# Optimization experiments

Measured on AMD Instinct MI355X. Metric: run time of the kernel, lower is better.

## Reference

```python
import jax, jax.numpy as jnp
import numpy as np

B, C, H, W, HEADS, S = 8, 512, 32, 32, 8, 77
CH = C // HEADS  # per-head channels = 64
GROUPS = 32      # GroupNorm32


def setup_inputs() -> dict:
    key = jax.random.key(0)
    ks = jax.random.split(key, 6)
    s = 0.02
    return {
        "x": jax.random.normal(ks[0], (B, C, H, W), jnp.float32),
        "encoder_out": jax.random.normal(ks[1], (B, C, S), jnp.float32),
        "capt_attn_mask": jax.random.bernoulli(ks[2], 0.9, (B, S)),
        "norm_scale": jnp.ones((C,), jnp.float32),
        "norm_bias": jnp.zeros((C,), jnp.float32),
        "qkv_w": jax.random.normal(ks[3], (3 * C, C), jnp.float32) * s,
        "qkv_b": jnp.zeros((3 * C,), jnp.float32),
        "ekv_w": jax.random.normal(ks[4], (2 * C, C), jnp.float32) * s,
        "ekv_b": jnp.zeros((2 * C,), jnp.float32),
        "proj_w": jax.random.normal(ks[5], (C, C), jnp.float32) * s,
        "proj_b": jnp.zeros((C,), jnp.float32),
    }


def reference(x, encoder_out, capt_attn_mask, norm_scale, norm_bias,
              qkv_w, qkv_b, ekv_w, ekv_b, proj_w, proj_b):
    b, c, h, w = x.shape
    T = h * w
    xf = x.reshape(b, c, T)

    # GroupNorm(32) in fp32 (GroupNorm32), affine
    xg = xf.reshape(b, GROUPS, c // GROUPS, T).astype(jnp.float32)
    mu = xg.mean(axis=(2, 3), keepdims=True)
    var = xg.var(axis=(2, 3), keepdims=True)
    nrm = ((xg - mu) * jax.lax.rsqrt(var + 1e-5)).reshape(b, c, T)
    nrm = nrm * norm_scale[None, :, None] + norm_bias[None, :, None]

    # 1x1 conv1d qkv projection: [b, 3c, T]
    qkv = jnp.einsum('oc,bct->bot', qkv_w, nrm) + qkv_b[None, :, None]
    qkv = qkv.reshape(b * HEADS, 3 * CH, T)
    q, k, v = jnp.split(qkv, 3, axis=1)  # each [b*heads, CH, T]

    # encoder kv: [b, 2c, S] -> [b*heads, 2*CH, S]
    ekv = jnp.einsum('oc,bcs->bos', ekv_w, encoder_out) + ekv_b[None, :, None]
    ekv = ekv.reshape(b * HEADS, 2 * CH, S)
    ek, ev = jnp.split(ekv, 2, axis=1)
    k = jnp.concatenate([ek, k], axis=-1)  # [b*heads, CH, S+T]
    v = jnp.concatenate([ev, v], axis=-1)

    scale = 1.0 / np.sqrt(np.sqrt(CH))
    wgt = jnp.einsum('bct,bcs->bts', q * scale, k * scale).astype(jnp.float32)

    # additive mask; torch.tile over dim0 is head-major (row i -> batch i % b),
    # faithfully reproduced; self-attn part (last T cols) is all-visible.
    addm_capt = jnp.where(jnp.tile(capt_attn_mask, (HEADS, 1)), 0.0, -10000.0)
    addm = jnp.concatenate(
        [addm_capt, jnp.zeros((b * HEADS, T), jnp.float32)], axis=1)[:, None, :]
    wgt = jax.nn.softmax(wgt + addm, axis=-1).astype(v.dtype)

    out = jnp.einsum('bts,bcs->bct', wgt, v)  # [b*heads, CH, T]
    out = out.reshape(b, c, T)
    out = jnp.einsum('oc,bct->bot', proj_w, out) + proj_b[None, :, None]
    return (xf + out).reshape(b, c, h, w)
```

## Files before the change

kernel.cpp:

```cpp
#include <hip/hip_runtime.h>
#include <math.h>

#define BB 8
#define TT 1024
#define SS 77

typedef short v8s __attribute__((ext_vector_type(8)));
typedef float v4f __attribute__((ext_vector_type(4)));
typedef unsigned short u16x4 __attribute__((ext_vector_type(4)));
typedef unsigned short u16x8 __attribute__((ext_vector_type(8)));
typedef unsigned short u16;

#define SCALEF 0.424660891f
#define MASKNEG (-14426.95f)

__device__ __forceinline__ u16 f2bf(float f) {
  unsigned u = __float_as_uint(f);
  u = (u + 0x7fffu + ((u >> 16) & 1u)) >> 16;
  return (u16)u;
}
__device__ __forceinline__ u16 hi16(float f) {
  return (u16)(__float_as_uint(f) >> 16);
}
__device__ __forceinline__ float bf2f(u16 u) {
  return __uint_as_float(((unsigned)u) << 16);
}
__device__ __forceinline__ void gl_lds16(const void* g, void* l) {
  __builtin_amdgcn_global_load_lds(
      (const __attribute__((address_space(1))) void*)g,
      (__attribute__((address_space(3))) void*)l, 16, 0, 0);
}

__global__ __launch_bounds__(256) void prep_gn_kernel(
    const float* __restrict__ x, const float* __restrict__ scale,
    const float* __restrict__ bias, u16* __restrict__ nrmT,
    const float* __restrict__ qkv_w, const float* __restrict__ ekv_w,
    const float* __restrict__ proj_w, const float* __restrict__ enc,
    const float* __restrict__ qkv_b, const float* __restrict__ ekv_b,
    u16* __restrict__ wQK, u16* __restrict__ wV, u16* __restrict__ wEK,
    u16* __restrict__ wEV, u16* __restrict__ projwb, u16* __restrict__ encT,
    float* __restrict__ bQK, float* __restrict__ bV,
    float* __restrict__ bEK, float* __restrict__ bEV) {
  __shared__ u16 Xs[16 * 1024];
  __shared__ float red[8];
  int blk = blockIdx.x, tid = threadIdx.x;

  if (blk < 256) {
    int bg = blk;
    int b = bg >> 5, g = bg & 31;
    const float4* x4 = (const float4*)(x + (size_t)bg * 16384);
    float s = 0.f, sq = 0.f;
#pragma unroll
    for (int i = 0; i < 16; ++i) {
      int idx = tid + 256 * i;
      float4 v = x4[idx];
      s += v.x + v.y + v.z + v.w;
      sq += v.x * v.x + v.y * v.y + v.z * v.z + v.w * v.w;
      int c = idx >> 8, t4 = (idx & 255) * 4;
      u16x4 o; o.x = f2bf(v.x); o.y = f2bf(v.y); o.z = f2bf(v.z); o.w = f2bf(v.w);
      *(u16x4*)(Xs + c * 1024 + t4) = o;
    }
#pragma unroll
    for (int off = 32; off > 0; off >>= 1) {
      s += __shfl_down(s, off, 64);
      sq += __shfl_down(sq, off, 64);
    }
    int wave = tid >> 6;
    if ((tid & 63) == 0) { red[wave] = s; red[wave + 4] = sq; }
    __syncthreads();
    float ts = red[0] + red[1] + red[2] + red[3];
    float tq = red[4] + red[5] + red[6] + red[7];
    float mu = ts * (1.0f / 16384.0f);
    float var = tq * (1.0f / 16384.0f) - mu * mu;
    float rs = rsqrtf(var + 1e-5f);
    float scv[16], biv[16];
#pragma unroll
    for (int c = 0; c < 16; ++c) {
      float ss = scale[g * 16 + c] * rs;
      scv[c] = ss;
      biv[c] = bias[g * 16 + c] - mu * ss;
    }
#pragma unroll
    for (int j = 0; j < 4; ++j) {
      int t = tid + 256 * j;
      u16x8 o0, o1;
#pragma unroll
      for (int c = 0; c < 8; ++c)  o0[c] = f2bf(bf2f(Xs[c * 1024 + t]) * scv[c] + biv[c]);
#pragma unroll
      for (int c = 8; c < 16; ++c) o1[c - 8] = f2bf(bf2f(Xs[c * 1024 + t]) * scv[c] + biv[c]);
      u16* dst = nrmT + ((size_t)b * 1024 + t) * 512 + g * 16;
      *(u16x8*)dst = o0;
      *(u16x8*)(dst + 8) = o1;
    }
    return;
  }

  int p = blk - 256;
  if (p < 512) {
    int idx = p * 256 + tid;
    int n = idx >> 7, c4 = (idx & 127) * 4;
    int which = n >> 9, h = (n >> 6) & 7, ch = n & 63;
    int src = h * 192 + which * 64 + ch;
    float4 v = *(const float4*)(qkv_w + (size_t)src * 512 + c4);
    u16x4 o; o.x = f2bf(v.x * SCALEF); o.y = f2bf(v.y * SCALEF);
    o.z = f2bf(v.z * SCALEF); o.w = f2bf(v.w * SCALEF);
    *(u16x4*)(wQK + (size_t)n * 512 + c4) = o;
  } else if (p < 768) {
    int idx = (p - 512) * 256 + tid;
    int n = idx >> 7, c4 = (idx & 127) * 4;
    int h = n >> 6, ch = n & 63;
    int src = h * 192 + 128 + ch;
    float4 v = *(const float4*)(qkv_w + (size_t)src * 512 + c4);
    u16x4 o; o.x = f2bf(v.x); o.y = f2bf(v.y); o.z = f2bf(v.z); o.w = f2bf(v.w);
    *(u16x4*)(wV + (size_t)n * 512 + c4) = o;
  } else if (p < 1024) {
    int idx = (p - 768) * 256 + tid;
    int n = idx >> 7, c4 = (idx & 127) * 4;
    int h = n >> 6, ch = n & 63;
    int src = h * 128 + ch;
    float4 v = *(const float4*)(ekv_w + (size_t)src * 512 + c4);
    u16x4 o; o.x = f2bf(v.x * SCALEF); o.y = f2bf(v.y * SCALEF);
    o.z = f2bf(v.z * SCALEF); o.w = f2bf(v.w * SCALEF);
    *(u16x4*)(wEK + (size_t)n * 512 + c4) = o;
  } else if (p < 1280) {
    int idx = (p - 1024) * 256 + tid;
    int n = idx >> 7, c4 = (idx & 127) * 4;
    int h = n >> 6, ch = n & 63;
    int src = h * 128 + 64 + ch;
    float4 v = *(const float4*)(ekv_w + (size_t)src * 512 + c4);
    u16x4 o; o.x = f2bf(v.x); o.y = f2bf(v.y); o.z = f2bf(v.z); o.w = f2bf(v.w);
    *(u16x4*)(wEV + (size_t)n * 512 + c4) = o;
  } else if (p < 1536) {
    int idx = (p - 1280) * 256 + tid;
    float4 v = ((const float4*)proj_w)[idx];
    u16x4 o; o.x = f2bf(v.x); o.y = f2bf(v.y); o.z = f2bf(v.z); o.w = f2bf(v.w);
    *(u16x4*)(projwb + (size_t)idx * 4) = o;
  } else if (p < 2048) {
    int idx = (p - 1536) * 256 + tid;
    int b = idx >> 14, rem = idx & 16383;
    int s = rem >> 7, c = (rem & 127) * 4;
    u16x4 o; o.x = 0; o.y = 0; o.z = 0; o.w = 0;
    if (s < SS) {
      const float* pp = enc + ((size_t)b * 512 + c) * SS + s;
      o.x = f2bf(pp[0]); o.y = f2bf(pp[SS]); o.z = f2bf(pp[2 * SS]); o.w = f2bf(pp[3 * SS]);
    }
    *(u16x4*)(encT + ((size_t)b * 128 + s) * 512 + c) = o;
  } else {
    for (int i = tid; i < 2560; i += 256) {
      if (i < 1024) {
        int which = i >> 9, h = (i >> 6) & 7, ch = i & 63;
        bQK[i] = qkv_b[h * 192 + which * 64 + ch] * SCALEF;
      } else if (i < 1536) {
        int j = i - 1024; int h = j >> 6, ch = j & 63;
        bV[j] = qkv_b[h * 192 + 128 + ch];
      } else if (i < 2048) {
        int j = i - 1536; int h = j >> 6, ch = j & 63;
        bEK[j] = ekv_b[h * 128 + ch] * SCALEF;
      } else {
        int j = i - 2048; int h = j >> 6, ch = j & 63;
        bEV[j] = ekv_b[h * 128 + 64 + ch];
      }
    }
  }
}

__global__ __launch_bounds__(256) void proj_all(
    const u16* __restrict__ nrmT, const u16* __restrict__ encT,
    const u16* __restrict__ wQK, const u16* __restrict__ wEK,
    const u16* __restrict__ wV, const u16* __restrict__ wEV,
    const float* __restrict__ bQK, const float* __restrict__ bEK,
    const float* __restrict__ bV, const float* __restrict__ bEV,
    u16* __restrict__ Qh, u16* __restrict__ Kfull, u16* __restrict__ Vfull) {
  __shared__ __align__(16) u16 SH[24576];
  u16* As = SH;
  u16* Bs = SH + 12288;

  int jj = blockIdx.x, bz = blockIdx.y;
  int job = (jj & 7) * 13 + (jj >> 3);
  int tid = threadIdx.x;
  int lane = tid & 63, w = tid >> 6;
  int lan15 = lane & 15, quad = lane >> 4;
  int wm = w >> 1, wn = w & 1;

  int mode, m0, n0;
  const u16 *Ap, *Bp;
  const float* bias;
  u16 *dA = nullptr, *dB = nullptr;
  int TrA = 0, offA = 0, TrB = 0, offB = 0;
  int coff = 0;

  if (job < 64) {
    mode = 3; m0 = (job >> 3) * 128; n0 = (job & 7) * 128;
    Ap = nrmT + (size_t)bz * 1024 * 512; Bp = wQK; bias = bQK;
    dA = Qh; TrA = 1024; offA = 0; dB = Kfull; TrB = 1152; offB = 128;
  } else if (job < 68) {
    mode = 3; m0 = 0; n0 = (job - 64) * 128;
    Ap = encT + (size_t)bz * 128 * 512; Bp = wEK; bias = bEK;
    dA = Kfull; TrA = 1152; offA = 0; dB = Kfull; TrB = 1152; offB = 0;
  } else if (job < 100) {
    int jx = job - 68; mode = 0; m0 = (jx >> 3) * 128; n0 = (jx & 7) * 128;
    Ap = wV; Bp = nrmT + (size_t)bz * 1024 * 512; bias = bV;
    coff = 128;
  } else {
    int jx = job - 100; mode = 0; m0 = jx * 128; n0 = 0;
    Ap = wEV; Bp = encT + (size_t)bz * 128 * 512; bias = bEV;
    coff = 0;
  }

  int arow = lane >> 2;
  int fr = (arow & 3) ^ ((arow >> 2) & 3);
  int achk = (lane & 3) ^ fr;
  const char* Ag = (const char*)(Ap + (size_t)(m0 + w * 32 + arow) * 512) + achk * 16;
  const char* Bg = (const char*)(Bp + (size_t)(n0 + w * 32 + arow) * 512) + achk * 16;

#define PSTAGE(s, b) do { int kb_ = (s) * 64;                                  \
    gl_lds16(Ag + kb_,         (char*)As + (b) * 8192 + w * 2048);             \
    gl_lds16(Ag + kb_ + 16384, (char*)As + (b) * 8192 + w * 2048 + 1024);      \
    gl_lds16(Bg + kb_,         (char*)Bs + (b) * 8192 + w * 2048);             \
    gl_lds16(Bg + kb_ + 16384, (char*)Bs + (b) * 8192 + w * 2048 + 1024); } while (0)

  v4f acc[4][4] = {};

  PSTAGE(0, 0);
  PSTAGE(1, 1);
  asm volatile("s_waitcnt vmcnt(4)" ::: "memory");
  __builtin_amdgcn_sched_barrier(0);
  __builtin_amdgcn_s_barrier();
  __builtin_amdgcn_sched_barrier(0);

  int ch = (quad ^ (lan15 & 3) ^ ((lan15 >> 2) & 3)) * 16;
  int cur = 0;
  for (int s = 0; s < 16; ++s) {
    if (s <= 13) { int nb = cur + 2; if (nb >= 3) nb -= 3; PSTAGE(s + 2, nb); }
    const char* Ab = (const char*)As + cur * 8192;
    const char* Bb = (const char*)Bs + cur * 8192;
    v8s a[4], bf[4];
#pragma unroll
    for (int i = 0; i < 4; ++i)
      a[i] = *(const v8s*)(Ab + (wm * 64 + i * 16 + lan15) * 64 + ch);
#pragma unroll
    for (int j = 0; j < 4; ++j)
      bf[j] = *(const v8s*)(Bb + (wn * 64 + j * 16 + lan15) * 64 + ch);
    __builtin_amdgcn_s_setprio(1);
#pragma unroll
    for (int i = 0; i < 4; ++i)
#pragma unroll
      for (int j = 0; j < 4; ++j)
        acc[i][j] = __builtin_amdgcn_mfma_f32_16x16x32_bf16(a[i], bf[j], acc[i][j], 0, 0, 0);
    __builtin_amdgcn_s_setprio(0);
    if (s < 15) {
      if (s <= 13) asm volatile("s_waitcnt vmcnt(4)" ::: "memory");
      else         asm volatile("s_waitcnt vmcnt(0)" ::: "memory");
      __builtin_amdgcn_sched_barrier(0);
      __builtin_amdgcn_s_barrier();
      __builtin_amdgcn_sched_barrier(0);
    }
    cur = cur + 1; if (cur == 3) cur = 0;
  }
#undef PSTAGE

  if (mode == 3) {
    u16* Tr = SH;
    for (int ph = 0; ph < 2; ++ph) {
      __syncthreads();
      if (wn == ph) {
#pragma unroll
        for (int j = 0; j < 4; ++j) {
          int n = n0 + wn * 64 + j * 16 + lan15;
          float bv_ = bias[n];
#pragma unroll
          for (int i = 0; i < 4; ++i)
#pragma unroll
            for (int r = 0; r < 4; ++r)
              Tr[(wm * 64 + i * 16 + quad * 4 + r) * 72 + j * 16 + lan15] =
                  f2bf(acc[i][j][r] + bv_);
        }
      }
      __syncthreads();
      int nb = n0 + ph * 64;
      u16* dst = (nb < 512) ? dA : dB;
      int Trows = (nb < 512) ? TrA : TrB;
      int roff  = (nb < 512) ? offA : offB;
      int hh = (nb & 511) >> 6;
      int row = tid >> 1, seg = (tid & 1) * 32;
      u16* dp = dst + ((size_t)(bz * 8 + hh) * Trows + roff + m0 + row) * 64 + seg;
#pragma unroll
      for (int g = 0; g < 4; ++g)
        *(u16x8*)(dp + g * 8) = *(const u16x8*)(Tr + row * 72 + seg + g * 8);
    }
  } else {
    u16* Tr = SH;
    u16* Cb = Vfull + (size_t)bz * 512 * 1152;
    for (int ph = 0; ph < 2; ++ph) {
      __syncthreads();
      if (wn == ph) {
#pragma unroll
        for (int i = 0; i < 4; ++i) {
          int ob = wm * 64 + i * 16 + quad * 4;
#pragma unroll
          for (int r = 0; r < 4; ++r) {
            float bi = bias[m0 + ob + r];
#pragma unroll
            for (int j = 0; j < 4; ++j)
              Tr[(ob + r) * 72 + j * 16 + lan15] = f2bf(acc[i][j][r] + bi);
          }
        }
      }
      __syncthreads();
      int row = tid >> 1, seg = (tid & 1) * 32;
      u16* dp = Cb + (size_t)(m0 + row) * 1152 + coff + n0 + ph * 64 + seg;
#pragma unroll
      for (int g = 0; g < 4; ++g)
        *(u16x8*)(dp + g * 8) = *(const u16x8*)(Tr + row * 72 + seg + g * 8);
    }
  }
}

__global__ __launch_bounds__(256) void proj_out(
    const u16* __restrict__ A, const u16* __restrict__ B,
    const float* __restrict__ bias, const float* __restrict__ res,
    float* __restrict__ Cf) {
  __shared__ __align__(16) u16 SH[18432];
  u16* As = SH;
  u16* Bs = SH + 6144;

  int tid = threadIdx.x;
  int lane = tid & 63, w = tid >> 6;
  int lan15 = lane & 15, quad = lane >> 4;
  int wm = w >> 1, wn = w & 1;
  int m0 = blockIdx.y * 64, n0 = blockIdx.x * 128;
  int bz = blockIdx.z;
  const u16* Bb = B + (size_t)bz * 1024 * 512;

  int arow = lane >> 2;
  int fr = (arow & 3) ^ ((arow >> 2) & 3);
  int achk = (lane & 3) ^ fr;
  const char* Ag = (const char*)(A + (size_t)(m0 + w * 16 + arow) * 512) + achk * 16;
  const char* Bg = (const char*)(Bb + (size_t)(n0 + w * 32 + arow) * 512) + achk * 16;

#define OSTAGE(s, b) do { int kb_ = (s) * 64;                                  \
    gl_lds16(Ag + kb_,         (char*)As + (b) * 4096 + w * 1024);             \
    gl_lds16(Bg + kb_,         (char*)Bs + (b) * 8192 + w * 2048);             \
    gl_lds16(Bg + kb_ + 16384, (char*)Bs + (b) * 8192 + w * 2048 + 1024); } while (0)

  v4f acc[2][4] = {};

  OSTAGE(0, 0);
  OSTAGE(1, 1);
  asm volatile("s_waitcnt vmcnt(3)" ::: "memory");
  __builtin_amdgcn_sched_barrier(0);
  __builtin_amdgcn_s_barrier();
  __builtin_amdgcn_sched_barrier(0);

  int ch = (quad ^ (lan15 & 3) ^ ((lan15 >> 2) & 3)) * 16;
  int cur = 0;
  for (int s = 0; s < 16; ++s) {
    if (s <= 13) { int nb = cur + 2; if (nb >= 3) nb -= 3; OSTAGE(s + 2, nb); }
    const char* Ab = (const char*)As + cur * 4096;
    const char* Bbuf = (const char*)Bs + cur * 8192;
    v8s a[2], bf[4];
#pragma unroll
    for (int i = 0; i < 2; ++i)
      a[i] = *(const v8s*)(Ab + (wm * 32 + i * 16 + lan15) * 64 + ch);
#pragma unroll
    for (int j = 0; j < 4; ++j)
      bf[j] = *(const v8s*)(Bbuf + (wn * 64 + j * 16 + lan15) * 64 + ch);
    __builtin_amdgcn_s_setprio(1);
#pragma unroll
    for (int i = 0; i < 2; ++i)
#pragma unroll
      for (int j = 0; j < 4; ++j)
        acc[i][j] = __builtin_amdgcn_mfma_f32_16x16x32_bf16(a[i], bf[j], acc[i][j], 0, 0, 0);
    __builtin_amdgcn_s_setprio(0);
    if (s < 15) {
      if (s <= 13) asm volatile("s_waitcnt vmcnt(3)" ::: "memory");
      else         asm volatile("s_waitcnt vmcnt(0)" ::: "memory");
      __builtin_amdgcn_sched_barrier(0);
      __builtin_amdgcn_s_barrier();
      __builtin_amdgcn_sched_barrier(0);
    }
    cur = cur + 1; if (cur == 3) cur = 0;
  }
#undef OSTAGE

  const float* rb = res + (size_t)bz * 512 * 1024;
  float* Cb = Cf + (size_t)bz * 512 * 1024;
#pragma unroll
  for (int i = 0; i < 2; ++i) {
    int ob = m0 + wm * 32 + i * 16 + quad * 4;
#pragma unroll
    for (int r = 0; r < 4; ++r) {
      int o = ob + r;
      float bi = bias[o];
#pragma unroll
      for (int j = 0; j < 4; ++j) {
        int n = n0 + wn * 64 + j * 16 + lan15;
        Cb[(size_t)o * 1024 + n] = acc[i][j][r] + bi + rb[(size_t)o * 1024 + n];
      }
    }
  }
}

#define AOFF_K 0
#define AOFF_V 16384
#define AOFF_P 32768
#define AOFF_AM 51200
#define ASMEM  51712

__global__ __launch_bounds__(256) void attn_kernel(
    const u16* __restrict__ Qh, const u16* __restrict__ Kf,
    const u16* __restrict__ Vf, const int* __restrict__ mask,
    u16* __restrict__ attnT) {
  __shared__ __align__(16) unsigned char smem[ASMEM];
  float* AM = (float*)(smem + AOFF_AM);

  int bh = blockIdx.x, b = bh >> 3, h = bh & 7;
  int t0 = blockIdx.y * 128;
  int tid = threadIdx.x;
  int lane = tid & 63, w = tid >> 6;
  int lan15 = lane & 15, quad = lane >> 4;
  int r8 = lane >> 3, c8 = lane & 7;
  int swE = (c8 ^ r8) * 8;

  const u16* Qb = Qh + (size_t)bh * 1024 * 64;
  const u16* Kb = Kf + (size_t)bh * 1152 * 64;
  const u16* Vb = Vf + (size_t)bh * 64 * 1152;
  char* Pw = (char*)smem + AOFF_P + w * 4608;
  u16* Pu = (u16*)Pw;

  if (tid < 128)
    AM[tid] = (tid < SS) ? ((mask[h * SS + tid] != 0) ? 0.f : MASKNEG) : -1e30f;

#pragma unroll
  for (int i = 0; i < 4; ++i)
    gl_lds16(Qb + (size_t)(t0 + w * 32 + i * 8 + r8) * 64 + swE, Pw + i * 1024);
#pragma unroll
  for (int i = 0; i < 2; ++i) {
    int row = w * 16 + i * 8;
    gl_lds16(Kb + (size_t)(row + r8) * 64 + swE, (char*)smem + AOFF_K + row * 128);
    gl_lds16(Vb + (size_t)(row + r8) * 1152 + swE, (char*)smem + AOFF_V + row * 128);
  }
  __syncthreads();

  v8s aq[2][2];
#pragma unroll
  for (int mt = 0; mt < 2; ++mt)
#pragma unroll
    for (int ks = 0; ks < 2; ++ks)
      aq[mt][ks] = *(const v8s*)(Pw + (mt * 16 + lan15) * 128 +
                                 (((ks * 4 + quad) ^ (lan15 & 7)) * 16));

  v4f O[2][4] = {};
  float lsum[2] = {0.f, 0.f};

  for (int c = 0; c < 18; ++c) {
    int cur = c & 1;
    if (c < 17) {
      int nb = cur ^ 1;
#pragma unroll
      for (int i = 0; i < 2; ++i) {
        int row = w * 16 + i * 8;
        gl_lds16(Kb + (size_t)((c + 1) * 64 + row + r8) * 64 + swE,
                 (char*)smem + AOFF_K + nb * 8192 + row * 128);
        gl_lds16(Vb + (size_t)(row + r8) * 1152 + (c + 1) * 64 + swE,
                 (char*)smem + AOFF_V + nb * 8192 + row * 128);
      }
    }
    const char* Kc = (const char*)smem + AOFF_K + cur * 8192;
    const char* Vc = (const char*)smem + AOFF_V + cur * 8192;

    v4f ST[4][2] = {};
#pragma unroll
    for (int ks = 0; ks < 2; ++ks) {
      int cofs = ((ks * 4 + quad) ^ (lan15 & 7)) * 16;
      v8s bk[4];
#pragma unroll
      for (int nt = 0; nt < 4; ++nt)
        bk[nt] = *(const v8s*)(Kc + (nt * 16 + lan15) * 128 + cofs);
#pragma unroll
      for (int nt = 0; nt < 4; ++nt)
#pragma unroll
        for (int mt = 0; mt < 2; ++mt)
          ST[nt][mt] = __builtin_amdgcn_mfma_f32_16x16x32_bf16(bk[nt], aq[mt][ks], ST[nt][mt], 0, 0, 0);
    }

    if (c < 2) {
#pragma unroll
      for (int nt = 0; nt < 4; ++nt)
#pragma unroll
        for (int r = 0; r < 4; ++r) {
          float a_ = AM[c * 64 + nt * 16 + quad * 4 + r];
#pragma unroll
          for (int mt = 0; mt < 2; ++mt) ST[nt][mt][r] += a_;
        }
    }

#pragma unroll
    for (int mt = 0; mt < 2; ++mt) {
#pragma unroll
      for (int nt = 0; nt < 4; ++nt) {
        float e0 = __builtin_amdgcn_exp2f(ST[nt][mt][0]);
        float e1 = __builtin_amdgcn_exp2f(ST[nt][mt][1]);
        float e2 = __builtin_amdgcn_exp2f(ST[nt][mt][2]);
        float e3 = __builtin_amdgcn_exp2f(ST[nt][mt][3]);
        u16x4 pk; pk.x = hi16(e0); pk.y = hi16(e1); pk.z = hi16(e2); pk.w = hi16(e3);
        *(u16x4*)&Pu[(mt * 16 + lan15) * 72 + nt * 16 + quad * 4] = pk;
        lsum[mt] += (e0 + e1) + (e2 + e3);
      }
    }

#pragma unroll
    for (int ks = 0; ks < 2; ++ks) {
      int cofs = ((ks * 4 + quad) ^ (lan15 & 7)) * 16;
      v8s ap[2], bv[4];
#pragma unroll
      for (int mt = 0; mt < 2; ++mt)
        ap[mt] = *(const v8s*)(Pw + (mt * 16 + lan15) * 144 + ks * 64 + quad * 16);
#pragma unroll
      for (int nc = 0; nc < 4; ++nc)
        bv[nc] = *(const v8s*)(Vc + (nc * 16 + lan15) * 128 + cofs);
#pragma unroll
      for (int mt = 0; mt < 2; ++mt)
#pragma unroll
        for (int nc = 0; nc < 4; ++nc)
          O[mt][nc] = __builtin_amdgcn_mfma_f32_16x16x32_bf16(ap[mt], bv[nc], O[mt][nc], 0, 0, 0);
    }
    __syncthreads();
  }

#pragma unroll
  for (int mt = 0; mt < 2; ++mt) {
    float v = lsum[mt];
    v += __shfl_xor(v, 16, 64);
    v += __shfl_xor(v, 32, 64);
    AM[w * 32 + mt * 16 + lan15] = v;
  }
  __syncthreads();
  float inv[2][4];
#pragma unroll
  for (int mt = 0; mt < 2; ++mt)
#pragma unroll
    for (int r = 0; r < 4; ++r)
      inv[mt][r] = 1.0f / AM[w * 32 + mt * 16 + quad * 4 + r];

  float* Ot = (float*)smem;
#pragma unroll
  for (int mt = 0; mt < 2; ++mt)
#pragma unroll
    for (int nc = 0; nc < 4; ++nc)
#pragma unroll
      for (int r = 0; r < 4; ++r)
        Ot[(w * 32 + mt * 16 + quad * 4 + r) * 68 + nc * 16 + lan15] =
            O[mt][nc][r] * inv[mt][r];
  __syncthreads();
  {
    int row = tid >> 1, seg = (tid & 1) * 32;
    const float* src = Ot + row * 68 + seg;
    u16* dp = attnT + ((size_t)b * 1024 + t0 + row) * 512 + h * 64 + seg;
#pragma unroll
    for (int g = 0; g < 4; ++g) {
      u16x8 o;
#pragma unroll
      for (int k = 0; k < 8; ++k) o[k] = f2bf(src[g * 8 + k]);
      *(u16x8*)(dp + g * 8) = o;
    }
  }
}

extern "C" void kernel_launch(void* const* d_in, const int* in_sizes, int n_in,
                              void* d_out, int out_size, void* d_ws, size_t ws_size,
                              hipStream_t stream) {
  const float* x       = (const float*)d_in[0];
  const float* enc     = (const float*)d_in[1];
  const int*   mask    = (const int*)d_in[2];
  const float* nscale  = (const float*)d_in[3];
  const float* nbias   = (const float*)d_in[4];
  const float* qkv_w   = (const float*)d_in[5];
  const float* qkv_b   = (const float*)d_in[6];
  const float* ekv_w   = (const float*)d_in[7];
  const float* ekv_b   = (const float*)d_in[8];
  const float* proj_w  = (const float*)d_in[9];
  const float* proj_b  = (const float*)d_in[10];
  float* out = (float*)d_out;

  char* ws = (char*)d_ws;
  const size_t MiB = 1048576;
  u16* nrmT   = (u16*)(ws);
  u16* Qh     = (u16*)(ws + 8 * MiB);
  u16* Kfull  = (u16*)(ws + 16 * MiB);
  u16* Vfull  = (u16*)(ws + 26 * MiB);
  u16* attnT  = (u16*)(ws + 36 * MiB);
  u16* encT   = (u16*)(ws + 44 * MiB);
  u16* wQK    = (u16*)(ws + 45 * MiB);
  u16* wV     = (u16*)(ws + 46 * MiB);
  u16* wEK    = (u16*)(ws + 46 * MiB + 524288);
  u16* wEV    = (u16*)(ws + 47 * MiB);
  u16* projwb = (u16*)(ws + 47 * MiB + 524288);
  float* bQK  = (float*)(ws + 48 * MiB);
  float* bV   = (float*)(ws + 48 * MiB + 4096);
  float* bEK  = (float*)(ws + 48 * MiB + 6144);
  float* bEV  = (float*)(ws + 48 * MiB + 8192);

  prep_gn_kernel<<<dim3(2305), dim3(256), 0, stream>>>(
      x, nscale, nbias, nrmT, qkv_w, ekv_w, proj_w, enc, qkv_b, ekv_b,
      wQK, wV, wEK, wEV, projwb, encT, bQK, bV, bEK, bEV);

  proj_all<<<dim3(104, BB), dim3(256), 0, stream>>>(
      nrmT, encT, wQK, wEK, wV, wEV, bQK, bEK, bV, bEV, Qh, Kfull, Vfull);

  attn_kernel<<<dim3(64, 8), dim3(256), 0, stream>>>(
      Qh, Kfull, Vfull, mask, attnT);

  proj_out<<<dim3(8, 8, BB), dim3(256), 0, stream>>>(
      projwb, attnT, proj_b, x, out);
}
```

Before: 166.9 us.

## Store GEMM operands in K-blocked pre-swizzled layout for contiguous LDS loads

All bf16 GEMM operands (normalized activations, weights, encoder transpose, attention output) are now written by their producers in a K-chunk-major layout of 32-element slabs with the XOR bank swizzle already applied. The GEMM kernels' global-to-LDS loads then read contiguous 1KB runs per wave instead of strided 64-byte pieces from 1KB-apart rows. This aims to improve global load coalescing in the projection and output GEMMs. In exchange the producer stores become more scattered, and every producer and consumer must agree on the new layout.

```diff
diff --git a/kernel.cpp b/kernel.cpp
--- a/kernel.cpp
+++ b/kernel.cpp
@@ -13,6 +13,8 @@
 
 #define SCALEF 0.424660891f
 #define MASKNEG (-14426.95f)
+
+#define FR(r) ((((r) & 3) ^ (((r) >> 2) & 3)))
 
 __device__ __forceinline__ u16 f2bf(float f) {
   unsigned u = __float_as_uint(f);
@@ -88,9 +90,10 @@
       for (int c = 0; c < 8; ++c)  o0[c] = f2bf(bf2f(Xs[c * 1024 + t]) * scv[c] + biv[c]);
 #pragma unroll
       for (int c = 8; c < 16; ++c) o1[c - 8] = f2bf(bf2f(Xs[c * 1024 + t]) * scv[c] + biv[c]);
-      u16* dst = nrmT + ((size_t)b * 1024 + t) * 512 + g * 16;
-      *(u16x8*)dst = o0;
-      *(u16x8*)(dst + 8) = o1;
+      int frt = FR(t);
+      u16* dst = nrmT + (((size_t)b * 16 + (g >> 1)) * 1024 + t) * 32;
+      *(u16x8*)(dst + ((((g & 1) * 2) ^ frt) * 8)) = o0;
+      *(u16x8*)(dst + ((((g & 1) * 2 + 1) ^ frt) * 8)) = o1;
     }
     return;
   }
@@ -104,7 +107,8 @@
     float4 v = *(const float4*)(qkv_w + (size_t)src * 512 + c4);
     u16x4 o; o.x = f2bf(v.x * SCALEF); o.y = f2bf(v.y * SCALEF);
     o.z = f2bf(v.z * SCALEF); o.w = f2bf(v.w * SCALEF);
-    *(u16x4*)(wQK + (size_t)n * 512 + c4) = o;
+    int sl = ((((c4 & 31) >> 3) ^ FR(n)) * 8) + (c4 & 7);
+    *(u16x4*)(wQK + ((size_t)(c4 >> 5) * 1024 + n) * 32 + sl) = o;
   } else if (p < 768) {
     int idx = (p - 512) * 256 + tid;
     int n = idx >> 7, c4 = (idx & 127) * 4;
@@ -112,7 +116,8 @@
     int src = h * 192 + 128 + ch;
     float4 v = *(const float4*)(qkv_w + (size_t)src * 512 + c4);
     u16x4 o; o.x = f2bf(v.x); o.y = f2bf(v.y); o.z = f2bf(v.z); o.w = f2bf(v.w);
-    *(u16x4*)(wV + (size_t)n * 512 + c4) = o;
+    int sl = ((((c4 & 31) >> 3) ^ FR(n)) * 8) + (c4 & 7);
+    *(u16x4*)(wV + ((size_t)(c4 >> 5) * 512 + n) * 32 + sl) = o;
   } else if (p < 1024) {
     int idx = (p - 768) * 256 + tid;
     int n = idx >> 7, c4 = (idx & 127) * 4;
@@ -121,7 +126,8 @@
     float4 v = *(const float4*)(ekv_w + (size_t)src * 512 + c4);
     u16x4 o; o.x = f2bf(v.x * SCALEF); o.y = f2bf(v.y * SCALEF);
     o.z = f2bf(v.z * SCALEF); o.w = f2bf(v.w * SCALEF);
-    *(u16x4*)(wEK + (size_t)n * 512 + c4) = o;
+    int sl = ((((c4 & 31) >> 3) ^ FR(n)) * 8) + (c4 & 7);
+    *(u16x4*)(wEK + ((size_t)(c4 >> 5) * 512 + n) * 32 + sl) = o;
   } else if (p < 1280) {
     int idx = (p - 1024) * 256 + tid;
     int n = idx >> 7, c4 = (idx & 127) * 4;
@@ -129,12 +135,15 @@
     int src = h * 128 + 64 + ch;
     float4 v = *(const float4*)(ekv_w + (size_t)src * 512 + c4);
     u16x4 o; o.x = f2bf(v.x); o.y = f2bf(v.y); o.z = f2bf(v.z); o.w = f2bf(v.w);
-    *(u16x4*)(wEV + (size_t)n * 512 + c4) = o;
+    int sl = ((((c4 & 31) >> 3) ^ FR(n)) * 8) + (c4 & 7);
+    *(u16x4*)(wEV + ((size_t)(c4 >> 5) * 512 + n) * 32 + sl) = o;
   } else if (p < 1536) {
     int idx = (p - 1280) * 256 + tid;
-    float4 v = ((const float4*)proj_w)[idx];
+    int row = idx >> 7, c4 = (idx & 127) * 4;
+    float4 v = *(const float4*)(proj_w + (size_t)row * 512 + c4);
     u16x4 o; o.x = f2bf(v.x); o.y = f2bf(v.y); o.z = f2bf(v.z); o.w = f2bf(v.w);
-    *(u16x4*)(projwb + (size_t)idx * 4) = o;
+    int sl = ((((c4 & 31) >> 3) ^ FR(row)) * 8) + (c4 & 7);
+    *(u16x4*)(projwb + ((size_t)(c4 >> 5) * 512 + row) * 32 + sl) = o;
   } else if (p < 2048) {
     int idx = (p - 1536) * 256 + tid;
     int b = idx >> 14, rem = idx & 16383;
@@ -144,7 +153,8 @@
       const float* pp = enc + ((size_t)b * 512 + c) * SS + s;
       o.x = f2bf(pp[0]); o.y = f2bf(pp[SS]); o.z = f2bf(pp[2 * SS]); o.w = f2bf(pp[3 * SS]);
     }
-    *(u16x4*)(encT + ((size_t)b * 128 + s) * 512 + c) = o;
+    int sl = ((((c & 31) >> 3) ^ FR(s)) * 8) + (c & 7);
+    *(u16x4*)(encT + (((size_t)b * 16 + (c >> 5)) * 128 + s) * 32 + sl) = o;
   } else {
     for (int i = tid; i < 2560; i += 256) {
       if (i < 1024) {
@@ -182,7 +192,7 @@
   int lan15 = lane & 15, quad = lane >> 4;
   int wm = w >> 1, wn = w & 1;
 
-  int mode, m0, n0;
+  int mode, m0, n0, RA, RB;
   const u16 *Ap, *Bp;
   const float* bias;
   u16 *dA = nullptr, *dB = nullptr;
@@ -191,33 +201,31 @@
 
   if (job < 64) {
     mode = 3; m0 = (job >> 3) * 128; n0 = (job & 7) * 128;
-    Ap = nrmT + (size_t)bz * 1024 * 512; Bp = wQK; bias = bQK;
+    Ap = nrmT + (size_t)bz * 524288; RA = 1024; Bp = wQK; RB = 1024; bias = bQK;
     dA = Qh; TrA = 1024; offA = 0; dB = Kfull; TrB = 1152; offB = 128;
   } else if (job < 68) {
     mode = 3; m0 = 0; n0 = (job - 64) * 128;
-    Ap = encT + (size_t)bz * 128 * 512; Bp = wEK; bias = bEK;
+    Ap = encT + (size_t)bz * 65536; RA = 128; Bp = wEK; RB = 512; bias = bEK;
     dA = Kfull; TrA = 1152; offA = 0; dB = Kfull; TrB = 1152; offB = 0;
   } else if (job < 100) {
     int jx = job - 68; mode = 0; m0 = (jx >> 3) * 128; n0 = (jx & 7) * 128;
-    Ap = wV; Bp = nrmT + (size_t)bz * 1024 * 512; bias = bV;
+    Ap = wV; RA = 512; Bp = nrmT + (size_t)bz * 524288; RB = 1024; bias = bV;
     coff = 128;
   } else {
     int jx = job - 100; mode = 0; m0 = jx * 128; n0 = 0;
-    Ap = wEV; Bp = encT + (size_t)bz * 128 * 512; bias = bEV;
+    Ap = wEV; RA = 512; Bp = encT + (size_t)bz * 65536; RB = 128; bias = bEV;
     coff = 0;
   }
 
-  int arow = lane >> 2;
-  int fr = (arow & 3) ^ ((arow >> 2) & 3);
-  int achk = (lane & 3) ^ fr;
-  const char* Ag = (const char*)(Ap + (size_t)(m0 + w * 32 + arow) * 512) + achk * 16;
-  const char* Bg = (const char*)(Bp + (size_t)(n0 + w * 32 + arow) * 512) + achk * 16;
-
-#define PSTAGE(s, b) do { int kb_ = (s) * 64;                                  \
-    gl_lds16(Ag + kb_,         (char*)As + (b) * 8192 + w * 2048);             \
-    gl_lds16(Ag + kb_ + 16384, (char*)As + (b) * 8192 + w * 2048 + 1024);      \
-    gl_lds16(Bg + kb_,         (char*)Bs + (b) * 8192 + w * 2048);             \
-    gl_lds16(Bg + kb_ + 16384, (char*)Bs + (b) * 8192 + w * 2048 + 1024); } while (0)
+  const char* Ag = (const char*)Ap + ((size_t)(m0 + w * 32) * 64) + lane * 16;
+  const char* Bg = (const char*)Bp + ((size_t)(n0 + w * 32) * 64) + lane * 16;
+  size_t astr = (size_t)RA * 64, bstr = (size_t)RB * 64;
+
+#define PSTAGE(s, b) do {                                                      \
+    gl_lds16(Ag + (size_t)(s) * astr,        (char*)As + (b) * 8192 + w * 2048);\
+    gl_lds16(Ag + (size_t)(s) * astr + 1024, (char*)As + (b) * 8192 + w * 2048 + 1024);\
+    gl_lds16(Bg + (size_t)(s) * bstr,        (char*)Bs + (b) * 8192 + w * 2048);\
+    gl_lds16(Bg + (size_t)(s) * bstr + 1024, (char*)Bs + (b) * 8192 + w * 2048 + 1024); } while (0)
 
   v4f acc[4][4] = {};
 
@@ -228,7 +236,7 @@
   __builtin_amdgcn_s_barrier();
   __builtin_amdgcn_sched_barrier(0);
 
-  int ch = (quad ^ (lan15 & 3) ^ ((lan15 >> 2) & 3)) * 16;
+  int ch = (quad ^ FR(lan15)) * 16;
   int cur = 0;
   for (int s = 0; s < 16; ++s) {
     if (s <= 13) { int nb = cur + 2; if (nb >= 3) nb -= 3; PSTAGE(s + 2, nb); }
@@ -330,18 +338,16 @@
   int wm = w >> 1, wn = w & 1;
   int m0 = blockIdx.y * 64, n0 = blockIdx.x * 128;
   int bz = blockIdx.z;
-  const u16* Bb = B + (size_t)bz * 1024 * 512;
-
-  int arow = lane >> 2;
-  int fr = (arow & 3) ^ ((arow >> 2) & 3);
-  int achk = (lane & 3) ^ fr;
-  const char* Ag = (const char*)(A + (size_t)(m0 + w * 16 + arow) * 512) + achk * 16;
-  const char* Bg = (const char*)(Bb + (size_t)(n0 + w * 32 + arow) * 512) + achk * 16;
-
-#define OSTAGE(s, b) do { int kb_ = (s) * 64;                                  \
-    gl_lds16(Ag + kb_,         (char*)As + (b) * 4096 + w * 1024);             \
-    gl_lds16(Bg + kb_,         (char*)Bs + (b) * 8192 + w * 2048);             \
-    gl_lds16(Bg + kb_ + 16384, (char*)Bs + (b) * 8192 + w * 2048 + 1024); } while (0)
+  const u16* Bb = B + (size_t)bz * 524288;
+
+  const char* Ag = (const char*)A + ((size_t)(m0 + w * 16) * 64) + lane * 16;
+  const char* Bg = (const char*)Bb + ((size_t)(n0 + w * 32) * 64) + lane * 16;
+  const size_t astr = 512 * 64, bstr = 1024 * 64;
+
+#define OSTAGE(s, b) do {                                                      \
+    gl_lds16(Ag + (size_t)(s) * astr,        (char*)As + (b) * 4096 + w * 1024);\
+    gl_lds16(Bg + (size_t)(s) * bstr,        (char*)Bs + (b) * 8192 + w * 2048);\
+    gl_lds16(Bg + (size_t)(s) * bstr + 1024, (char*)Bs + (b) * 8192 + w * 2048 + 1024); } while (0)
 
   v4f acc[2][4] = {};
 
@@ -352,7 +358,7 @@
   __builtin_amdgcn_s_barrier();
   __builtin_amdgcn_sched_barrier(0);
 
-  int ch = (quad ^ (lan15 & 3) ^ ((lan15 >> 2) & 3)) * 16;
+  int ch = (quad ^ FR(lan15)) * 16;
   int cur = 0;
   for (int s = 0; s < 16; ++s) {
     if (s <= 13) { int nb = cur + 2; if (nb >= 3) nb -= 3; OSTAGE(s + 2, nb); }
@@ -554,15 +560,16 @@
             O[mt][nc][r] * inv[mt][r];
   __syncthreads();
   {
-    int row = tid >> 1, seg = (tid & 1) * 32;
-    const float* src = Ot + row * 68 + seg;
-    u16* dp = attnT + ((size_t)b * 1024 + t0 + row) * 512 + h * 64 + seg;
+    int row = tid >> 1, ks2 = tid & 1;
+    const float* src = Ot + row * 68 + ks2 * 32;
+    int frt = FR(row);
+    u16* dpn = attnT + (((size_t)b * 16 + h * 2 + ks2) * 1024 + t0 + row) * 32;
 #pragma unroll
     for (int g = 0; g < 4; ++g) {
       u16x8 o;
 #pragma unroll
       for (int k = 0; k < 8; ++k) o[k] = f2bf(src[g * 8 + k]);
-      *(u16x8*)(dp + g * 8) = o;
+      *(u16x8*)(dpn + ((g ^ frt) * 8)) = o;
     }
   }
 }
```

New measurement: 165.8 us, median of 3. Within noise of the previous version (-0.6%).
